# Optimization experiments

Hardware: AMD Instinct MI355X
Metric: run time of the kernel (lower is better)

Reference implementation:

```python
import jax, jax.numpy as jnp
import numpy as np

NUM_AGENTS = 1000
N_ACTIONS = 16
HIDDEN = 256
COMM_STEPS = 4
B, M = 1024, 64


def setup_inputs() -> dict:
    key = jax.random.key(0)
    ks = jax.random.split(key, 8)
    agent_ids = jax.random.randint(ks[0], (B, M), 0, NUM_AGENTS)
    emb = jax.random.normal(ks[1], (NUM_AGENTS, HIDDEN), dtype=jnp.float32) * 0.1
    s1 = 1.0 / np.sqrt(3 * HIDDEN)
    W1 = jax.random.uniform(ks[2], (3 * HIDDEN, HIDDEN), jnp.float32, -s1, s1)
    b1 = jax.random.uniform(ks[3], (HIDDEN,), jnp.float32, -s1, s1)
    s2 = 1.0 / np.sqrt(HIDDEN)
    W2 = jax.random.uniform(ks[4], (HIDDEN, HIDDEN), jnp.float32, -s2, s2)
    b2 = jax.random.uniform(ks[5], (HIDDEN,), jnp.float32, -s2, s2)
    Wd = jax.random.uniform(ks[6], (HIDDEN, N_ACTIONS), jnp.float32, -s2, s2)
    bd = jax.random.uniform(ks[7], (N_ACTIONS,), jnp.float32, -s2, s2)
    return {"agent_ids": agent_ids, "emb": emb, "W1": W1, "b1": b1,
            "W2": W2, "b2": b2, "Wd": Wd, "bd": bd}


def reference(agent_ids, emb, W1, b1, W2, b2, Wd, bd):
    # h0: (B, M, H) embedding lookup
    h0 = emb[agent_ids]
    h = h0
    m = agent_ids.shape[1]
    inv = 1.0 / (m - 1)
    for _ in range(COMM_STEPS):
        # mean of other agents' hidden states: c_j = (sum_k h_k - h_j)/(M-1)
        c = (jnp.sum(h, axis=1, keepdims=True) - h) * inv
        x = jnp.concatenate([h, c, h0], axis=-1)  # (B, M, 3H)
        delta = jax.nn.relu(jnp.einsum('bmi,ih->bmh', x, W1) + b1)
        delta = jnp.einsum('bmi,ih->bmh', delta, W2) + b2
        h = h + delta  # residual (use_skip=True)
    logits = jnp.einsum('bmh,ha->bma', h, Wd) + bd
    return logits
```

## Files before the change

kernel.cpp:

```cpp
#include <hip/hip_runtime.h>

#define HID 256
#define NB 1024
#define NACT 16

typedef __bf16 bf16x8 __attribute__((ext_vector_type(8)));
typedef float  f32x4  __attribute__((ext_vector_type(4)));

#define HA_LO   32768
#define OV      65536
#define LDS_TOT 81920

#define PREP_N (4 * 65536 + 4096)

__device__ __forceinline__ unsigned short f2bf(float x) {
    union { float f; unsigned u; } v; v.f = x;
    unsigned r = v.u + 0x7fff + ((v.u >> 16) & 1);
    return (unsigned short)(r >> 16);
}
__device__ __forceinline__ float bf2f(unsigned short b) {
    union { float f; unsigned u; } v; v.u = ((unsigned)b) << 16;
    return v.f;
}
__device__ __forceinline__ float b2f_lo(unsigned v) { return bf2f((unsigned short)(v & 0xffffu)); }
__device__ __forceinline__ float b2f_hi(unsigned v) { return bf2f((unsigned short)(v >> 16)); }

__global__ __launch_bounds__(256) void prep_k(const float* __restrict__ W1,
                                              const float* __restrict__ W2,
                                              const float* __restrict__ Wd,
                                              unsigned short* __restrict__ WAh, unsigned short* __restrict__ WAl,
                                              unsigned short* __restrict__ WHh, unsigned short* __restrict__ WHl,
                                              unsigned short* __restrict__ WBh, unsigned short* __restrict__ WBl,
                                              unsigned short* __restrict__ WDh, unsigned short* __restrict__ WDl,
                                              float* __restrict__ Wc) {
    int i = blockIdx.x * 256 + threadIdx.x;
    const float inv = 1.0f / 63.0f;
    if (i < 3 * 65536) {
        int mat = i >> 16, j = i & 65535;
        int kq = j >> 13, r = j & 8191;
        int nb = r >> 9, r2 = r & 511;
        int l = r2 >> 3, e = r2 & 7;
        int n = nb * 16 + (l & 15);
        int k = kq * 32 + (l >> 4) * 8 + e;
        float val;
        if (mat == 0)      val = W1[k * 256 + n] - inv * W1[(256 + k) * 256 + n];
        else if (mat == 1) val = W1[(512 + k) * 256 + n];
        else               val = W2[k * 256 + n];
        unsigned short hi = f2bf(val);
        unsigned short lo = f2bf(val - bf2f(hi));
        if (mat == 0)      { WAh[j] = hi; WAl[j] = lo; }
        else if (mat == 1) { WHh[j] = hi; WHl[j] = lo; }
        else               { WBh[j] = hi; WBl[j] = lo; }
    } else if (i < 4 * 65536) {
        int j = i - 3 * 65536, k = j >> 8, n = j & 255;
        Wc[j] = inv * W1[(256 + k) * 256 + n];
    } else if (i < PREP_N) {
        int j = i - 4 * 65536, a = j >> 8, k = j & 255;
        float val = Wd[k * 16 + a];
        unsigned short hi = f2bf(val);
        WDh[j] = hi; WDl[j] = f2bf(val - bf2f(hi));
    }
}

__device__ __forceinline__ void kloopL2(const unsigned short* __restrict__ Wfh,
                                        const unsigned short* __restrict__ Wfl,
                                        const char* hA, f32x4 (&acc)[4][2],
                                        int w, int lane, int l15, int g)
{
    const int rxA = (l15 & 7) << 4;
    const size_t lbase = ((size_t)(w * 2) * 64 + lane) * 8;
    #pragma unroll 2
    for (int kq = 0; kq < 8; ++kq) {
        const int cb = (kq * 64 + g * 16) ^ rxA;
        bf16x8 ah[4], al[4];
        #pragma unroll
        for (int mt = 0; mt < 4; ++mt) {
            int rb = (mt * 16 + l15) * 512;
            ah[mt] = *(const bf16x8*)(hA + rb + cb);
            al[mt] = *(const bf16x8*)(hA + HA_LO + rb + cb);
        }
        const size_t kb = (size_t)kq * 8192 + lbase;
        #pragma unroll
        for (int nt = 0; nt < 2; ++nt) {
            bf16x8 bh = *(const bf16x8*)(Wfh + kb + nt * 512);
            bf16x8 bl = *(const bf16x8*)(Wfl + kb + nt * 512);
            #pragma unroll
            for (int mt = 0; mt < 4; ++mt) {
                acc[mt][nt] = __builtin_amdgcn_mfma_f32_16x16x32_bf16(ah[mt], bh, acc[mt][nt], 0, 0, 0);
                acc[mt][nt] = __builtin_amdgcn_mfma_f32_16x16x32_bf16(al[mt], bh, acc[mt][nt], 0, 0, 0);
                acc[mt][nt] = __builtin_amdgcn_mfma_f32_16x16x32_bf16(ah[mt], bl, acc[mt][nt], 0, 0, 0);
            }
        }
    }
}

__device__ __forceinline__ void STfun(char* lds, const float* __restrict__ Wc, int tid)
{
    char* hA = lds;
    float* Sp = (float*)(lds + OV);
    float* Sf = (float*)(lds + OV + 4096);
    float* Tp = (float*)(lds + OV + 8192);
    __syncthreads();
    {
        int ww = tid & 127, gq = tid >> 7;
        float s0 = 0.f, s1 = 0.f;
        #pragma unroll 4
        for (int m = gq * 16; m < gq * 16 + 16; ++m) {
            int byte = m * 512 + ((ww * 4) ^ ((m & 7) << 4));
            unsigned vh = *(const unsigned*)(hA + byte);
            unsigned vl = *(const unsigned*)(hA + HA_LO + byte);
            s0 += b2f_lo(vh) + b2f_lo(vl);
            s1 += b2f_hi(vh) + b2f_hi(vl);
        }
        Sp[gq * 256 + ww * 2] = s0;
        Sp[gq * 256 + ww * 2 + 1] = s1;
    }
    __syncthreads();
    if (tid < 256) Sf[tid] = (Sp[tid] + Sp[256 + tid]) + (Sp[512 + tid] + Sp[768 + tid]);
    __syncthreads();
    {
        int n = tid & 255, kh = tid >> 8;
        float a = 0.f;
        #pragma unroll 8
        for (int k = kh * 128; k < kh * 128 + 128; ++k)
            a += Sf[k] * Wc[(k << 8) + n];
        Tp[kh * 256 + n] = a;
    }
    __syncthreads();
}

__global__ __launch_bounds__(512, 2) void fused_all(
    const int* __restrict__ ids, const float* __restrict__ emb,
    const unsigned short* __restrict__ WAh, const unsigned short* __restrict__ WAl,
    const unsigned short* __restrict__ WHh, const unsigned short* __restrict__ WHl,
    const unsigned short* __restrict__ WBh, const unsigned short* __restrict__ WBl,
    const unsigned short* __restrict__ WDh, const unsigned short* __restrict__ WDl,
    const float* __restrict__ Wc,
    const float* __restrict__ b1, const float* __restrict__ b2,
    const float* __restrict__ bd, float* __restrict__ out)
{
    __shared__ __align__(16) char lds[LDS_TOT];
    const int tid = threadIdx.x;
    const int lane = tid & 63;
    const int w = tid >> 6;
    const int l15 = lane & 15, g = lane >> 4;
    const size_t rowbase = (size_t)blockIdx.x * 64;
    char* hA = lds;
    float* Tp = (float*)(lds + OV + 8192);

    {
        int r = tid >> 3, c0 = (tid & 7) * 32;
        int rx = (r & 7) << 4;
        const float4* src = (const float4*)(emb + (size_t)ids[rowbase + r] * HID + c0);
        char* dh = hA + r * 512;
        #pragma unroll
        for (int j = 0; j < 8; ++j) {
            float4 v = src[j];
            unsigned short h0 = f2bf(v.x), h1 = f2bf(v.y), h2 = f2bf(v.z), h3 = f2bf(v.w);
            unsigned short q0 = f2bf(v.x - bf2f(h0)), q1 = f2bf(v.y - bf2f(h1)),
                           q2 = f2bf(v.z - bf2f(h2)), q3 = f2bf(v.w - bf2f(h3));
            int byte = ((c0 + j * 4) * 2) ^ rx;
            *(uint2*)(dh + byte) = make_uint2((unsigned)h0 | ((unsigned)h1 << 16),
                                             (unsigned)h2 | ((unsigned)h3 << 16));
            *(uint2*)(dh + HA_LO + byte) = make_uint2((unsigned)q0 | ((unsigned)q1 << 16),
                                                      (unsigned)q2 | ((unsigned)q3 << 16));
        }
    }

    STfun(lds, Wc, tid);
    float tvr[2];
    #pragma unroll
    for (int nt = 0; nt < 2; ++nt) {
        int col = w * 32 + nt * 16 + l15;
        tvr[nt] = Tp[col] + Tp[256 + col];
    }

    f32x4 acc[4][2], u0r[4][2];
    #pragma unroll
    for (int mt = 0; mt < 4; ++mt)
        #pragma unroll
        for (int nt = 0; nt < 2; ++nt) acc[mt][nt] = (f32x4){0.f, 0.f, 0.f, 0.f};

    for (int s = 0; s < 4; ++s) {
        if (s == 0) {
            kloopL2(WHh, WHl, hA, acc, w, lane, l15, g);
            #pragma unroll
            for (int nt = 0; nt < 2; ++nt) {
                float bb = b1[w * 32 + nt * 16 + l15];
                #pragma unroll
                for (int mt = 0; mt < 4; ++mt)
                    #pragma unroll
                    for (int q = 0; q < 4; ++q) {
                        u0r[mt][nt][q] = acc[mt][nt][q] + bb;
                        acc[mt][nt][q] = 0.f;
                    }
            }
        }
        #pragma unroll
        for (int mt = 0; mt < 4; ++mt)
            #pragma unroll
            for (int nt = 0; nt < 2; ++nt)
                #pragma unroll
                for (int q = 0; q < 4; ++q)
                    acc[mt][nt][q] = tvr[nt] + u0r[mt][nt][q];
        kloopL2(WAh, WAl, hA, acc, w, lane, l15, g);

        __syncthreads();
        {
            float b2r0 = b2[w * 32 + l15], b2r1 = b2[w * 32 + 16 + l15];
            #pragma unroll
            for (int mt = 0; mt < 4; ++mt)
                #pragma unroll
                for (int nt = 0; nt < 2; ++nt)
                    #pragma unroll
                    for (int q = 0; q < 4; ++q) {
                        int row = mt * 16 + g * 4 + q;
                        int col = w * 32 + nt * 16 + l15;
                        int byte = row * 512 + ((col * 2) ^ ((row & 7) << 4));
                        float hres = bf2f(*(const unsigned short*)(hA + byte))
                                   + bf2f(*(const unsigned short*)(hA + HA_LO + byte));
                        float a = fmaxf(acc[mt][nt][q], 0.f);
                        unsigned short hi = f2bf(a);
                        *(unsigned short*)(hA + byte) = hi;
                        *(unsigned short*)(hA + HA_LO + byte) = f2bf(a - bf2f(hi));
                        acc[mt][nt][q] = hres + (nt ? b2r1 : b2r0);
                    }
        }
        __syncthreads();

        kloopL2(WBh, WBl, hA, acc, w, lane, l15, g);

        __syncthreads();
        #pragma unroll
        for (int mt = 0; mt < 4; ++mt)
            #pragma unroll
            for (int nt = 0; nt < 2; ++nt)
                #pragma unroll
                for (int q = 0; q < 4; ++q) {
                    int row = mt * 16 + g * 4 + q;
                    int col = w * 32 + nt * 16 + l15;
                    int byte = row * 512 + ((col * 2) ^ ((row & 7) << 4));
                    float hv = acc[mt][nt][q];
                    unsigned short hi = f2bf(hv);
                    *(unsigned short*)(hA + byte) = hi;
                    *(unsigned short*)(hA + HA_LO + byte) = f2bf(hv - bf2f(hi));
                    acc[mt][nt][q] = 0.f;
                }

        if (s < 3) {
            STfun(lds, Wc, tid);
            #pragma unroll
            for (int nt = 0; nt < 2; ++nt) {
                int col = w * 32 + nt * 16 + l15;
                tvr[nt] = Tp[col] + Tp[256 + col];
            }
        }
    }

    __syncthreads();
    {
        float* Dp = (float*)(lds + OV);
        if (w < 4) {
            f32x4 dacc[4];
            #pragma unroll
            for (int mi = 0; mi < 4; ++mi) dacc[mi] = (f32x4){0.f, 0.f, 0.f, 0.f};
            #pragma unroll
            for (int kh = 0; kh < 2; ++kh) {
                const int k = w * 64 + kh * 32;
                bf16x8 wdh = *(const bf16x8*)(WDh + (size_t)l15 * 256 + k + g * 8);
                bf16x8 wdl = *(const bf16x8*)(WDl + (size_t)l15 * 256 + k + g * 8);
                #pragma unroll
                for (int mi = 0; mi < 4; ++mi) {
                    int m = mi * 16 + l15;
                    int byte = m * 512 + ((k * 2 + g * 16) ^ ((m & 7) << 4));
                    bf16x8 hh = *(const bf16x8*)(hA + byte);
                    bf16x8 hl = *(const bf16x8*)(hA + HA_LO + byte);
                    dacc[mi] = __builtin_amdgcn_mfma_f32_16x16x32_bf16(wdh, hh, dacc[mi], 0, 0, 0);
                    dacc[mi] = __builtin_amdgcn_mfma_f32_16x16x32_bf16(wdl, hh, dacc[mi], 0, 0, 0);
                    dacc[mi] = __builtin_amdgcn_mfma_f32_16x16x32_bf16(wdh, hl, dacc[mi], 0, 0, 0);
                }
            }
            #pragma unroll
            for (int mi = 0; mi < 4; ++mi)
                #pragma unroll
                for (int q = 0; q < 4; ++q)
                    Dp[w * 1024 + (mi * 16 + l15) * 16 + g * 4 + q] = dacc[mi][q];
        }
    }
    __syncthreads();
    {
        float* Dp = (float*)(lds + OV);
        int m = tid >> 3, a0 = (tid & 7) * 2;
        float o0 = bd[a0], o1 = bd[a0 + 1];
        #pragma unroll
        for (int w4 = 0; w4 < 4; ++w4) {
            o0 += Dp[w4 * 1024 + m * 16 + a0];
            o1 += Dp[w4 * 1024 + m * 16 + a0 + 1];
        }
        *(float2*)(out + ((size_t)rowbase + m) * NACT + a0) = make_float2(o0, o1);
    }
}

extern "C" void kernel_launch(void* const* d_in, const int* in_sizes, int n_in,
                              void* d_out, int out_size, void* d_ws, size_t ws_size,
                              hipStream_t stream) {
    const int*   ids = (const int*)d_in[0];
    const float* emb = (const float*)d_in[1];
    const float* W1  = (const float*)d_in[2];
    const float* b1  = (const float*)d_in[3];
    const float* W2  = (const float*)d_in[4];
    const float* b2  = (const float*)d_in[5];
    const float* Wd  = (const float*)d_in[6];
    const float* bd  = (const float*)d_in[7];
    float* out = (float*)d_out;

    char* p = (char*)d_ws;
    unsigned short* WAh = (unsigned short*)p; p += 65536 * 2;
    unsigned short* WAl = (unsigned short*)p; p += 65536 * 2;
    unsigned short* WHh = (unsigned short*)p; p += 65536 * 2;
    unsigned short* WHl = (unsigned short*)p; p += 65536 * 2;
    unsigned short* WBh = (unsigned short*)p; p += 65536 * 2;
    unsigned short* WBl = (unsigned short*)p; p += 65536 * 2;
    unsigned short* WDh = (unsigned short*)p; p += 4096 * 2;
    unsigned short* WDl = (unsigned short*)p; p += 4096 * 2;
    float* Wc = (float*)p;

    prep_k<<<(PREP_N + 255) / 256, 256, 0, stream>>>(W1, W2, Wd, WAh, WAl, WHh, WHl,
                                                     WBh, WBl, WDh, WDl, Wc);
    fused_all<<<NB, 512, 0, stream>>>(ids, emb, WAh, WAl, WHh, WHl, WBh, WBl,
                                      WDh, WDl, Wc, b1, b2, bd, out);
}
```

Measured before the change: 273.4 us.

## Split decoder by rows across waves and shrink LDS footprint

The final logits projection now gives each of four waves a 16-row slice over the full K dimension and writes results straight to global memory. This replaces the previous K-split across waves, which needed an LDS partial-sum buffer, an extra barrier and a reduction pass. The LDS allocation shrinks accordingly, with the Tp scratch offset moved down. The bf16 conversion helpers now use native __bf16 casts instead of manual bit rounding. The epilogue is a small part of the kernel, and the LDS reduction may not change occupancy at two blocks per CU.

```diff
diff --git a/kernel.cpp b/kernel.cpp
--- a/kernel.cpp
+++ b/kernel.cpp
@@ -9,18 +9,15 @@
 
 #define HA_LO   32768
 #define OV      65536
-#define LDS_TOT 81920
+#define LDS_TOT 72704
 
 #define PREP_N (4 * 65536 + 4096)
 
 __device__ __forceinline__ unsigned short f2bf(float x) {
-    union { float f; unsigned u; } v; v.f = x;
-    unsigned r = v.u + 0x7fff + ((v.u >> 16) & 1);
-    return (unsigned short)(r >> 16);
-}
-__device__ __forceinline__ float bf2f(unsigned short b) {
-    union { float f; unsigned u; } v; v.u = ((unsigned)b) << 16;
-    return v.f;
+    union { __bf16 b; unsigned short u; } v; v.b = (__bf16)x; return v.u;
+}
+__device__ __forceinline__ float bf2f(unsigned short u) {
+    union { unsigned short u; __bf16 b; } v; v.u = u; return (float)v.b;
 }
 __device__ __forceinline__ float b2f_lo(unsigned v) { return bf2f((unsigned short)(v & 0xffffu)); }
 __device__ __forceinline__ float b2f_hi(unsigned v) { return bf2f((unsigned short)(v >> 16)); }
@@ -99,7 +96,7 @@
     char* hA = lds;
     float* Sp = (float*)(lds + OV);
     float* Sf = (float*)(lds + OV + 4096);
-    float* Tp = (float*)(lds + OV + 8192);
+    float* Tp = (float*)(lds + OV + 5120);
     __syncthreads();
     {
         int ww = tid & 127, gq = tid >> 7;
@@ -146,7 +143,7 @@
     const int l15 = lane & 15, g = lane >> 4;
     const size_t rowbase = (size_t)blockIdx.x * 64;
     char* hA = lds;
-    float* Tp = (float*)(lds + OV + 8192);
+    float* Tp = (float*)(lds + OV + 5120);
 
     {
         int r = tid >> 3, c0 = (tid & 7) * 32;
@@ -258,46 +255,25 @@
     }
 
     __syncthreads();
-    {
-        float* Dp = (float*)(lds + OV);
-        if (w < 4) {
-            f32x4 dacc[4];
-            #pragma unroll
-            for (int mi = 0; mi < 4; ++mi) dacc[mi] = (f32x4){0.f, 0.f, 0.f, 0.f};
-            #pragma unroll
-            for (int kh = 0; kh < 2; ++kh) {
-                const int k = w * 64 + kh * 32;
-                bf16x8 wdh = *(const bf16x8*)(WDh + (size_t)l15 * 256 + k + g * 8);
-                bf16x8 wdl = *(const bf16x8*)(WDl + (size_t)l15 * 256 + k + g * 8);
-                #pragma unroll
-                for (int mi = 0; mi < 4; ++mi) {
-                    int m = mi * 16 + l15;
-                    int byte = m * 512 + ((k * 2 + g * 16) ^ ((m & 7) << 4));
-                    bf16x8 hh = *(const bf16x8*)(hA + byte);
-                    bf16x8 hl = *(const bf16x8*)(hA + HA_LO + byte);
-                    dacc[mi] = __builtin_amdgcn_mfma_f32_16x16x32_bf16(wdh, hh, dacc[mi], 0, 0, 0);
-                    dacc[mi] = __builtin_amdgcn_mfma_f32_16x16x32_bf16(wdl, hh, dacc[mi], 0, 0, 0);
-                    dacc[mi] = __builtin_amdgcn_mfma_f32_16x16x32_bf16(wdh, hl, dacc[mi], 0, 0, 0);
-                }
-            }
-            #pragma unroll
-            for (int mi = 0; mi < 4; ++mi)
-                #pragma unroll
-                for (int q = 0; q < 4; ++q)
-                    Dp[w * 1024 + (mi * 16 + l15) * 16 + g * 4 + q] = dacc[mi][q];
-        }
-    }
-    __syncthreads();
-    {
-        float* Dp = (float*)(lds + OV);
-        int m = tid >> 3, a0 = (tid & 7) * 2;
-        float o0 = bd[a0], o1 = bd[a0 + 1];
-        #pragma unroll
-        for (int w4 = 0; w4 < 4; ++w4) {
-            o0 += Dp[w4 * 1024 + m * 16 + a0];
-            o1 += Dp[w4 * 1024 + m * 16 + a0 + 1];
-        }
-        *(float2*)(out + ((size_t)rowbase + m) * NACT + a0) = make_float2(o0, o1);
+    if (w < 4) {
+        const int rx = (l15 & 7) << 4;
+        const float bdv = bd[l15];
+        f32x4 dacc = (f32x4){0.f, 0.f, 0.f, 0.f};
+        #pragma unroll 2
+        for (int kq = 0; kq < 8; ++kq) {
+            int byte = (w * 16 + l15) * 512 + ((kq * 64 + g * 16) ^ rx);
+            bf16x8 hh = *(const bf16x8*)(hA + byte);
+            bf16x8 hl = *(const bf16x8*)(hA + HA_LO + byte);
+            const int k = kq * 32;
+            bf16x8 wdh = *(const bf16x8*)(WDh + (size_t)l15 * 256 + k + g * 8);
+            bf16x8 wdl = *(const bf16x8*)(WDl + (size_t)l15 * 256 + k + g * 8);
+            dacc = __builtin_amdgcn_mfma_f32_16x16x32_bf16(hh, wdh, dacc, 0, 0, 0);
+            dacc = __builtin_amdgcn_mfma_f32_16x16x32_bf16(hl, wdh, dacc, 0, 0, 0);
+            dacc = __builtin_amdgcn_mfma_f32_16x16x32_bf16(hh, wdl, dacc, 0, 0, 0);
+        }
+        #pragma unroll
+        for (int q = 0; q < 4; ++q)
+            out[(rowbase + w * 16 + g * 4 + q) * NACT + l15] = dacc[q] + bdv;
     }
 }
 
```

Measured after the change: 277.5 us. About the same (+1.5%).
